# Optimization experiments

Measured on AMD Instinct MI355X. Metric: run time of the kernel, lower is better.

## Reference

```python
import jax, jax.numpy as jnp
import numpy as np

N_OBS = 1_000_000
N_ROWS = 8192
N_COLS = 8192
RANK = 64


def setup_inputs() -> dict:
    key = jax.random.key(0)
    ks = jax.random.split(key, 7)
    vals = jax.random.normal(ks[0], (N_OBS,), dtype=jnp.float32)
    rows = jax.random.randint(ks[1], (N_OBS,), 0, N_ROWS)
    cols = jax.random.randint(ks[2], (N_OBS,), 0, N_COLS)
    stdv = 1.0 / np.sqrt(RANK)
    U = jax.random.uniform(ks[3], (N_ROWS, RANK), dtype=jnp.float32, minval=-stdv, maxval=stdv)
    V = jax.random.uniform(ks[4], (RANK, N_COLS), dtype=jnp.float32, minval=-stdv, maxval=stdv)
    sigma = jnp.ones((1,), dtype=jnp.float32)
    S_U = jax.random.normal(ks[5], (N_ROWS, N_ROWS), dtype=jnp.float32)
    S_V = jax.random.normal(ks[6], (N_COLS, N_COLS), dtype=jnp.float32)
    return {"vals": vals, "rows": rows, "cols": cols, "U": U, "V": V,
            "sigma": sigma, "S_U": S_U, "S_V": S_V}


def reference(vals, rows, cols, U, V, sigma, S_U, S_V):
    # Energy term: sum_n (t_n - U[i_n,:] . V[:,j_n])^2 / (2 sigma^2)
    u_rows = U[rows]              # [N, R] gather
    v_cols = V[:, cols].T         # [N, R] gather
    preds = jnp.einsum('nr,nr->n', u_rows, v_cols)  # [N]
    s2 = sigma[0] ** 2
    E = jnp.sum((vals - preds) ** 2) / (s2 * 2.0)
    # 0.5 * tr(U^T S_U U): per-rank quadratic forms batched into one contraction
    E = E + 0.5 * jnp.einsum('ir,ij,jr->', U, S_U, U)
    # 0.5 * tr(V S_V V^T): rows of V against S_V
    E = E + 0.5 * jnp.einsum('rn,nm,rm->', V, S_V, V)
    E = E + vals.shape[0] * jnp.log(s2)
    return E.reshape(1, 1)
```

## Files before the change

### kernel.cpp

```cpp
#include <hip/hip_runtime.h>
#include <math.h>

#define N_OBS_C  1000000
#define NDIM     8192
#define RANK_C   64

typedef __attribute__((ext_vector_type(8))) short bf16x8;
typedef __attribute__((ext_vector_type(4))) float f32x4;

__device__ __forceinline__ unsigned short f2bf(float f) {
  union { float f; unsigned int u; } x; x.f = f;
  unsigned int u = x.u;
  unsigned int r = (u + 0x7fffu + ((u >> 16) & 1u)) >> 16;
  return (unsigned short)r;
}

__global__ void prep_kernel(const float* __restrict__ V, const float* __restrict__ U,
                            float* __restrict__ Vt, unsigned short* __restrict__ Ub,
                            unsigned short* __restrict__ Vtb) {
  int b = blockIdx.x, t = threadIdx.x;
  if (b < 128) {
    __shared__ float tile[64][65];
    int c0 = b * 64;
#pragma unroll
    for (int i = 0; i < 16; ++i) {
      int idx = i * 256 + t;
      int r = idx >> 6, c = idx & 63;
      tile[r][c] = V[r * NDIM + c0 + c];
    }
    __syncthreads();
#pragma unroll
    for (int i = 0; i < 16; ++i) {
      int idx = i * 256 + t;
      int n = idx >> 6, r = idx & 63;
      float v = tile[r][n];
      Vt[(c0 + n) * RANK_C + r]  = v;
      Vtb[(c0 + n) * RANK_C + r] = f2bf(v);
    }
  } else {
    int nt  = 64 * 256;
    int tid = (b - 128) * 256 + t;
    for (int i = tid; i < NDIM * RANK_C; i += nt)
      Ub[i] = f2bf(U[i]);
  }
}

__device__ __forceinline__ void block_reduce_atomic(float v, float* out) {
#pragma unroll
  for (int off = 32; off > 0; off >>= 1) v += __shfl_down(v, off, 64);
  __shared__ float wsum[4];
  int w = threadIdx.x >> 6;
  if ((threadIdx.x & 63) == 0) wsum[w] = v;
  __syncthreads();
  if (threadIdx.x == 0) atomicAdd(out, wsum[0] + wsum[1] + wsum[2] + wsum[3]);
}

__global__ void __launch_bounds__(256, 2)
main_kernel(const float* __restrict__ vals, const int* __restrict__ rows,
            const int* __restrict__ cols, const float* __restrict__ U,
            const float* __restrict__ sigma, const float* __restrict__ S_U,
            const float* __restrict__ S_V, const float* __restrict__ Vt,
            const unsigned short* __restrict__ Ub,
            const unsigned short* __restrict__ Vtb, float* __restrict__ out) {
  const int E_BLOCKS = 2048;
  const int TILES_PER = 64 * 64;
  int bid = blockIdx.x;
  int t = threadIdx.x;

  __shared__ float gbuf[4][16][132];

  if (bid % 5 == 0) {
    int eb = bid / 5;
    float s2 = sigma[0] * sigma[0];
    float local = 0.f;
    int stride = E_BLOCKS * 256;
    for (int n = eb * 256 + t; n < N_OBS_C; n += stride) {
      int r = rows[n], c = cols[n];
      const f32x4* up = (const f32x4*)(U  + (size_t)r * RANK_C);
      const f32x4* vp = (const f32x4*)(Vt + (size_t)c * RANK_C);
      float d0 = 0.f, d1 = 0.f, d2 = 0.f, d3 = 0.f;
#pragma unroll
      for (int k = 0; k < 16; k += 4) {
        f32x4 a0 = up[k],     b0 = vp[k];
        f32x4 a1 = up[k + 1], b1 = vp[k + 1];
        f32x4 a2 = up[k + 2], b2 = vp[k + 2];
        f32x4 a3 = up[k + 3], b3 = vp[k + 3];
        d0 += a0[0]*b0[0] + a0[1]*b0[1] + a0[2]*b0[2] + a0[3]*b0[3];
        d1 += a1[0]*b1[0] + a1[1]*b1[1] + a1[2]*b1[2] + a1[3]*b1[3];
        d2 += a2[0]*b2[0] + a2[1]*b2[1] + a2[2]*b2[2] + a2[3]*b2[3];
        d3 += a3[0]*b3[0] + a3[1]*b3[1] + a3[2]*b3[2] + a3[3]*b3[3];
      }
      float e = vals[n] - ((d0 + d1) + (d2 + d3));
      local += e * e;
    }
    local *= 1.0f / (2.0f * s2);
    if (bid == 0 && t == 0) local += (float)N_OBS_C * logf(s2);
    block_reduce_atomic(local, out);
  } else {
    int sb = (bid / 5) * 4 + (bid % 5 - 1);
    const float* S; const unsigned short* A;
    if (sb < TILES_PER) { S = S_U; A = Ub; }
    else                { S = S_V; A = Vtb; sb -= TILES_PER; }
    int ti0 = (sb >> 6) * 128;
    int tj0 = (sb & 63) * 128;

    int w = t >> 6, lane = t & 63, quad = lane >> 4, lcol = lane & 15;

    bf16x8 af[2][2];
#pragma unroll
    for (int ti = 0; ti < 2; ++ti)
#pragma unroll
      for (int kh = 0; kh < 2; ++kh) {
        int row = ti0 + w * 32 + ti * 16 + lcol;
        af[ti][kh] = *(const bf16x8*)(A + (size_t)row * RANK_C + kh * 32 + quad * 8);
      }
    bf16x8 bfr[8][2];
#pragma unroll
    for (int tj = 0; tj < 8; ++tj)
#pragma unroll
      for (int kh = 0; kh < 2; ++kh) {
        int row = tj0 + tj * 16 + lcol;
        bfr[tj][kh] = *(const bf16x8*)(A + (size_t)row * RANK_C + kh * 32 + quad * 8);
      }

    f32x4 acc[2][8];
#pragma unroll
    for (int ti = 0; ti < 2; ++ti)
#pragma unroll
      for (int tj = 0; tj < 8; ++tj) {
        f32x4 z = {0.f, 0.f, 0.f, 0.f};
        z = __builtin_amdgcn_mfma_f32_16x16x32_bf16(af[ti][0], bfr[tj][0], z, 0, 0, 0);
        z = __builtin_amdgcn_mfma_f32_16x16x32_bf16(af[ti][1], bfr[tj][1], z, 0, 0, 0);
        acc[ti][tj] = z;
      }

    int h = lane >> 5, l31 = lane & 31;
    f32x4 Greg[16];
#pragma unroll
    for (int ti = 0; ti < 2; ++ti) {
#pragma unroll
      for (int tj = 0; tj < 8; ++tj)
#pragma unroll
        for (int reg = 0; reg < 4; ++reg)
          gbuf[w][quad * 4 + reg][tj * 16 + lcol] = acc[ti][tj][reg];
      __syncthreads();
#pragma unroll
      for (int i = 0; i < 8; ++i)
        Greg[ti * 8 + i] = *(const f32x4*)&gbuf[w][2 * i + h][4 * l31];
      __syncthreads();
    }

    const float* Sp = S + (size_t)(ti0 + w * 32 + h) * NDIM + tj0 + 4 * l31;
    f32x4 sv[16];
#pragma unroll
    for (int i = 0; i < 16; ++i)
      sv[i] = *(const f32x4*)(Sp + (size_t)(2 * i) * NDIM);
    f32x4 sum = {0.f, 0.f, 0.f, 0.f};
#pragma unroll
    for (int i = 0; i < 16; ++i) sum += sv[i] * Greg[i];
    float p = (sum[0] + sum[1]) + (sum[2] + sum[3]);
    block_reduce_atomic(0.5f * p, out);
  }
}

extern "C" void kernel_launch(void* const* d_in, const int* in_sizes, int n_in,
                              void* d_out, int out_size, void* d_ws, size_t ws_size,
                              hipStream_t stream) {
  const float* vals  = (const float*)d_in[0];
  const int*   rows  = (const int*)  d_in[1];
  const int*   cols  = (const int*)  d_in[2];
  const float* U     = (const float*)d_in[3];
  const float* V     = (const float*)d_in[4];
  const float* sigma = (const float*)d_in[5];
  const float* S_U   = (const float*)d_in[6];
  const float* S_V   = (const float*)d_in[7];
  float* out = (float*)d_out;

  char* ws = (char*)d_ws;
  float*          Vt  = (float*)ws;
  unsigned short* Ub  = (unsigned short*)(ws + 2u * 1024 * 1024);
  unsigned short* Vtb = (unsigned short*)(ws + 3u * 1024 * 1024);

  hipMemsetAsync(d_out, 0, sizeof(float), stream);
  prep_kernel<<<192, 256, 0, stream>>>(V, U, Vt, Ub, Vtb);
  main_kernel<<<10240, 256, 0, stream>>>(vals, rows, cols, U, sigma, S_U, S_V,
                                         Vt, Ub, Vtb, out);
}
```

Measured before the change: 590.6 us.

## Drop LDS transpose by swapping MFMA operands; loop over wider S tiles

The quadratic-form path swaps the MFMA operand order so the accumulator layout matches row-major S loads directly. This removes the shared-memory transpose and its two barriers. Each block now walks a 128x512 strip in eight chunks, which cuts the grid to 3072 blocks and raises launch_bounds occupancy to 4. The energy path software-prefetches the next index and value triple. The main risk is lower per-block parallelism and a serial inner loop that may expose S load latency.

Result: slower. 714.3 us (+20.9%).

```diff
diff --git a/kernel.cpp b/kernel.cpp
--- a/kernel.cpp
+++ b/kernel.cpp
@@ -4,6 +4,9 @@
 #define N_OBS_C  1000000
 #define NDIM     8192
 #define RANK_C   64
+
+#define E_BLOCKS 1024
+#define S_BLOCKS 2048
 
 typedef __attribute__((ext_vector_type(8))) short bf16x8;
 typedef __attribute__((ext_vector_type(4))) float f32x4;
@@ -55,109 +58,101 @@
   if (threadIdx.x == 0) atomicAdd(out, wsum[0] + wsum[1] + wsum[2] + wsum[3]);
 }
 
-__global__ void __launch_bounds__(256, 2)
+__global__ void __launch_bounds__(256, 4)
 main_kernel(const float* __restrict__ vals, const int* __restrict__ rows,
             const int* __restrict__ cols, const float* __restrict__ U,
             const float* __restrict__ sigma, const float* __restrict__ S_U,
             const float* __restrict__ S_V, const float* __restrict__ Vt,
             const unsigned short* __restrict__ Ub,
             const unsigned short* __restrict__ Vtb, float* __restrict__ out) {
-  const int E_BLOCKS = 2048;
-  const int TILES_PER = 64 * 64;
   int bid = blockIdx.x;
   int t = threadIdx.x;
 
-  __shared__ float gbuf[4][16][132];
-
-  if (bid % 5 == 0) {
-    int eb = bid / 5;
+  if (bid % 3 == 0) {
     float s2 = sigma[0] * sigma[0];
     float local = 0.f;
-    int stride = E_BLOCKS * 256;
-    for (int n = eb * 256 + t; n < N_OBS_C; n += stride) {
+    const int estride = E_BLOCKS * 256;
+    int n = (bid / 3) * 256 + t;
+    if (n < N_OBS_C) {
       int r = rows[n], c = cols[n];
-      const f32x4* up = (const f32x4*)(U  + (size_t)r * RANK_C);
-      const f32x4* vp = (const f32x4*)(Vt + (size_t)c * RANK_C);
-      float d0 = 0.f, d1 = 0.f, d2 = 0.f, d3 = 0.f;
+      float v = vals[n];
+      for (;;) {
+        int nn = n + estride;
+        bool more = (nn < N_OBS_C);
+        int rn = 0, cn = 0; float vn = 0.f;
+        if (more) { rn = rows[nn]; cn = cols[nn]; vn = vals[nn]; }
+
+        const f32x4* up = (const f32x4*)(U  + (size_t)r * RANK_C);
+        const f32x4* vp = (const f32x4*)(Vt + (size_t)c * RANK_C);
+        float d0 = 0.f, d1 = 0.f, d2 = 0.f, d3 = 0.f;
 #pragma unroll
-      for (int k = 0; k < 16; k += 4) {
-        f32x4 a0 = up[k],     b0 = vp[k];
-        f32x4 a1 = up[k + 1], b1 = vp[k + 1];
-        f32x4 a2 = up[k + 2], b2 = vp[k + 2];
-        f32x4 a3 = up[k + 3], b3 = vp[k + 3];
-        d0 += a0[0]*b0[0] + a0[1]*b0[1] + a0[2]*b0[2] + a0[3]*b0[3];
-        d1 += a1[0]*b1[0] + a1[1]*b1[1] + a1[2]*b1[2] + a1[3]*b1[3];
-        d2 += a2[0]*b2[0] + a2[1]*b2[1] + a2[2]*b2[2] + a2[3]*b2[3];
-        d3 += a3[0]*b3[0] + a3[1]*b3[1] + a3[2]*b3[2] + a3[3]*b3[3];
+        for (int k = 0; k < 16; k += 4) {
+          f32x4 a0 = up[k],     b0 = vp[k];
+          f32x4 a1 = up[k + 1], b1 = vp[k + 1];
+          f32x4 a2 = up[k + 2], b2 = vp[k + 2];
+          f32x4 a3 = up[k + 3], b3 = vp[k + 3];
+          d0 += a0[0]*b0[0] + a0[1]*b0[1] + a0[2]*b0[2] + a0[3]*b0[3];
+          d1 += a1[0]*b1[0] + a1[1]*b1[1] + a1[2]*b1[2] + a1[3]*b1[3];
+          d2 += a2[0]*b2[0] + a2[1]*b2[1] + a2[2]*b2[2] + a2[3]*b2[3];
+          d3 += a3[0]*b3[0] + a3[1]*b3[1] + a3[2]*b3[2] + a3[3]*b3[3];
+        }
+        float e = v - ((d0 + d1) + (d2 + d3));
+        local += e * e;
+        if (!more) break;
+        n = nn; r = rn; c = cn; v = vn;
       }
-      float e = vals[n] - ((d0 + d1) + (d2 + d3));
-      local += e * e;
     }
     local *= 1.0f / (2.0f * s2);
     if (bid == 0 && t == 0) local += (float)N_OBS_C * logf(s2);
     block_reduce_atomic(local, out);
   } else {
-    int sb = (bid / 5) * 4 + (bid % 5 - 1);
+    int sb = (bid / 3) * 2 + (bid % 3) - 1;
     const float* S; const unsigned short* A;
-    if (sb < TILES_PER) { S = S_U; A = Ub; }
-    else                { S = S_V; A = Vtb; sb -= TILES_PER; }
-    int ti0 = (sb >> 6) * 128;
-    int tj0 = (sb & 63) * 128;
+    if (sb < S_BLOCKS / 2) { S = S_U; A = Ub; }
+    else                   { S = S_V; A = Vtb; sb -= S_BLOCKS / 2; }
+    int ti0 = (sb >> 4) * 128;
+    int j0  = (sb & 15) * 512;
 
     int w = t >> 6, lane = t & 63, quad = lane >> 4, lcol = lane & 15;
+    int r0 = ti0 + w * 32;
 
     bf16x8 af[2][2];
 #pragma unroll
     for (int ti = 0; ti < 2; ++ti)
 #pragma unroll
-      for (int kh = 0; kh < 2; ++kh) {
-        int row = ti0 + w * 32 + ti * 16 + lcol;
-        af[ti][kh] = *(const bf16x8*)(A + (size_t)row * RANK_C + kh * 32 + quad * 8);
-      }
-    bf16x8 bfr[8][2];
+      for (int kh = 0; kh < 2; ++kh)
+        af[ti][kh] = *(const bf16x8*)(A + (size_t)(r0 + ti * 16 + lcol) * RANK_C +
+                                      kh * 32 + quad * 8);
+
+    const float* Sb = S + (size_t)(r0 + lcol) * NDIM + j0 + quad * 4;
+    f32x4 sum = {0.f, 0.f, 0.f, 0.f};
+
+#pragma unroll 1
+    for (int hh = 0; hh < 8; ++hh) {
+      int cb = j0 + hh * 64;
+      bf16x8 bfr[4][2];
 #pragma unroll
-    for (int tj = 0; tj < 8; ++tj)
+      for (int tj = 0; tj < 4; ++tj)
 #pragma unroll
-      for (int kh = 0; kh < 2; ++kh) {
-        int row = tj0 + tj * 16 + lcol;
-        bfr[tj][kh] = *(const bf16x8*)(A + (size_t)row * RANK_C + kh * 32 + quad * 8);
-      }
-
-    f32x4 acc[2][8];
+        for (int kh = 0; kh < 2; ++kh)
+          bfr[tj][kh] = *(const bf16x8*)(A + (size_t)(cb + tj * 16 + lcol) * RANK_C +
+                                         kh * 32 + quad * 8);
+      f32x4 sv[2][4];
 #pragma unroll
-    for (int ti = 0; ti < 2; ++ti)
+      for (int ti = 0; ti < 2; ++ti)
 #pragma unroll
-      for (int tj = 0; tj < 8; ++tj) {
-        f32x4 z = {0.f, 0.f, 0.f, 0.f};
-        z = __builtin_amdgcn_mfma_f32_16x16x32_bf16(af[ti][0], bfr[tj][0], z, 0, 0, 0);
-        z = __builtin_amdgcn_mfma_f32_16x16x32_bf16(af[ti][1], bfr[tj][1], z, 0, 0, 0);
-        acc[ti][tj] = z;
-      }
-
-    int h = lane >> 5, l31 = lane & 31;
-    f32x4 Greg[16];
+        for (int tj = 0; tj < 4; ++tj)
+          sv[ti][tj] = *(const f32x4*)(Sb + (size_t)(ti * 16) * NDIM + hh * 64 + tj * 16);
 #pragma unroll
-    for (int ti = 0; ti < 2; ++ti) {
+      for (int ti = 0; ti < 2; ++ti)
 #pragma unroll
-      for (int tj = 0; tj < 8; ++tj)
-#pragma unroll
-        for (int reg = 0; reg < 4; ++reg)
-          gbuf[w][quad * 4 + reg][tj * 16 + lcol] = acc[ti][tj][reg];
-      __syncthreads();
-#pragma unroll
-      for (int i = 0; i < 8; ++i)
-        Greg[ti * 8 + i] = *(const f32x4*)&gbuf[w][2 * i + h][4 * l31];
-      __syncthreads();
+        for (int tj = 0; tj < 4; ++tj) {
+          f32x4 z = {0.f, 0.f, 0.f, 0.f};
+          z = __builtin_amdgcn_mfma_f32_16x16x32_bf16(bfr[tj][0], af[ti][0], z, 0, 0, 0);
+          z = __builtin_amdgcn_mfma_f32_16x16x32_bf16(bfr[tj][1], af[ti][1], z, 0, 0, 0);
+          sum += z * sv[ti][tj];
+        }
     }
-
-    const float* Sp = S + (size_t)(ti0 + w * 32 + h) * NDIM + tj0 + 4 * l31;
-    f32x4 sv[16];
-#pragma unroll
-    for (int i = 0; i < 16; ++i)
-      sv[i] = *(const f32x4*)(Sp + (size_t)(2 * i) * NDIM);
-    f32x4 sum = {0.f, 0.f, 0.f, 0.f};
-#pragma unroll
-    for (int i = 0; i < 16; ++i) sum += sv[i] * Greg[i];
     float p = (sum[0] + sum[1]) + (sum[2] + sum[3]);
     block_reduce_atomic(0.5f * p, out);
   }
@@ -183,6 +178,6 @@
 
   hipMemsetAsync(d_out, 0, sizeof(float), stream);
   prep_kernel<<<192, 256, 0, stream>>>(V, U, Vt, Ub, Vtb);
-  main_kernel<<<10240, 256, 0, stream>>>(vals, rows, cols, U, sigma, S_U, S_V,
-                                         Vt, Ub, Vtb, out);
+  main_kernel<<<E_BLOCKS + S_BLOCKS, 256, 0, stream>>>(vals, rows, cols, U, sigma,
+                                                       S_U, S_V, Vt, Ub, Vtb, out);
 }
```
